# Optimization experiments

Hardware: AMD Instinct MI355X
Metric: run time of the kernel (lower is better)

The kernel has to match this reference:

```python
import jax, jax.numpy as jnp
import numpy as np

M, N = 4096, 4096

def _make_expk(n):
    k = np.arange(n, dtype=np.float64) * np.pi / (2.0 * n)
    return jnp.asarray(np.stack([np.cos(k), np.sin(k)], axis=-1), dtype=jnp.float32)

def setup_inputs() -> dict:
    key = jax.random.key(0)
    x = jax.random.normal(key, (M, N), dtype=jnp.float32)
    return {"x": x, "expkM": _make_expk(M), "expkN": _make_expk(N)}

def _idct_last(X, expk):
    """1D IDCT (inverse of unnormalized DCT-II) along last axis via Makhoul's
    N-point FFT trick. expk[k] = (cos, sin) of pi*k/(2N), i.e. e^{j pi k/(2N)}."""
    n = X.shape[-1]
    Xv = X * 0.5
    # V[k] = (Xv[k] - j*Xv[n-k]) * e^{j pi k/(2n)}, with imag part 0 at k=0
    tail = -jnp.flip(Xv, axis=-1)[..., :-1]
    Vi = jnp.concatenate([jnp.zeros_like(Xv[..., :1]), tail], axis=-1)
    W = expk[:, 0] + 1j * expk[:, 1]
    V = (Xv + 1j * Vi) * W
    v = jnp.fft.ifft(V, axis=-1).real.astype(X.dtype)
    # de-interleave: out[2m] = v[m], out[2m+1] = v[n-1-m]
    out = jnp.zeros_like(X)
    out = out.at[..., 0::2].set(v[..., : n - n // 2])
    out = out.at[..., 1::2].set(jnp.flip(v, axis=-1)[..., : n // 2])
    return out

def reference(x, expkM, expkN):
    # separable 2D IDCT: last axis (N) then first axis (M)
    y = _idct_last(x, expkN)
    y = _idct_last(y.T, expkM).T
    return y
```

## Files before the change

### kernel.cpp

```cpp
#include <hip/hip_runtime.h>
#include <math.h>


#define NN 4096
#define HH 2048
#define TT 256
#define PHYS(i) ((i) + ((i) >> 3))
#define C_SQ2 0.70710678118654752440f

__global__ void tw_init_kernel(float2* __restrict__ tw4096,
                               float2* __restrict__ tw2048) {
    int t = threadIdx.x;
    for (int i = 0; i < HH / TT; ++i) {
        int k = t + i * TT;
        double a4 = (2.0 * M_PI * (double)k) / 4096.0;
        double a2 = (2.0 * M_PI * (double)k) / 2048.0;
        tw4096[k] = make_float2((float)cos(a4), (float)sin(a4));
        tw2048[k] = make_float2((float)cos(a2), (float)sin(a2));
    }
}

__device__ __forceinline__ void radix8(const float* ar, const float* ai,
                                       float* tr, float* ti) {
    float s04r = ar[0] + ar[4], s04i = ai[0] + ai[4];
    float d04r = ar[0] - ar[4], d04i = ai[0] - ai[4];
    float s26r = ar[2] + ar[6], s26i = ai[2] + ai[6];
    float d26r = ar[2] - ar[6], d26i = ai[2] - ai[6];
    float E0r = s04r + s26r, E0i = s04i + s26i;
    float E1r = d04r - d26i, E1i = d04i + d26r;
    float E2r = s04r - s26r, E2i = s04i - s26i;
    float E3r = d04r + d26i, E3i = d04i - d26r;
    float s15r = ar[1] + ar[5], s15i = ai[1] + ai[5];
    float d15r = ar[1] - ar[5], d15i = ai[1] - ai[5];
    float s37r = ar[3] + ar[7], s37i = ai[3] + ai[7];
    float d37r = ar[3] - ar[7], d37i = ai[3] - ai[7];
    float O0r = s15r + s37r, O0i = s15i + s37i;
    float O1r = d15r - d37i, O1i = d15i + d37r;
    float O2r = s15r - s37r, O2i = s15i - s37i;
    float O3r = d15r + d37i, O3i = d15i - d37r;
    float W1r = C_SQ2 * (O1r - O1i), W1i = C_SQ2 * (O1r + O1i);
    float W2r = -O2i, W2i = O2r;
    float W3r = -C_SQ2 * (O3r + O3i), W3i = C_SQ2 * (O3r - O3i);
    tr[0] = E0r + O0r; ti[0] = E0i + O0i;
    tr[4] = E0r - O0r; ti[4] = E0i - O0i;
    tr[1] = E1r + W1r; ti[1] = E1i + W1i;
    tr[5] = E1r - W1r; ti[5] = E1i - W1i;
    tr[2] = E2r + W2r; ti[2] = E2i + W2i;
    tr[6] = E2r - W2r; ti[6] = E2i - W2i;
    tr[3] = E3r + W3r; ti[3] = E3i + W3i;
    tr[7] = E3r - W3r; ti[7] = E3i - W3i;
}

__global__ __launch_bounds__(TT) void idct_rows_kernel(
    const float* __restrict__ in, const float2* __restrict__ expk,
    const float2* __restrict__ tw4096, const float2* __restrict__ tw2048,
    float* __restrict__ out) {
    __shared__ float b0r[2304], b0i[2304], b1r[2304], b1i[2304];
    const int t = threadIdx.x;
    const float* __restrict__ xr = in + (size_t)blockIdx.x * NN;
    float* __restrict__ orow = out + (size_t)blockIdx.x * NN;
    const float sc = 1.0f / 4096.0f;

    float zr[8], zi[8];
#pragma unroll
    for (int p = 0; p < 8; ++p) {
        int k = t + TT * p;
        float xa = xr[k];
        float xb = xr[(NN - k) & (NN - 1)];
        xb = (k == 0) ? 0.0f : xb;
        float2 e1 = expk[k];
        float var_ = 0.5f * (xa * e1.x + xb * e1.y);
        float vai_ = 0.5f * (xa * e1.y - xb * e1.x);
        float xc = xr[k + HH];
        float xd = xr[HH - k];
        float2 e2 = expk[k + HH];
        float vbr_ = 0.5f * (xc * e2.x + xd * e2.y);
        float vbi_ = 0.5f * (xc * e2.y - xd * e2.x);
        float sr = var_ + vbr_, si = vai_ + vbi_;
        float dr = var_ - vbr_, di = vai_ - vbi_;
        float2 w = tw4096[k];
        zr[p] = (sr - (w.x * di + w.y * dr)) * sc;
        zi[p] = (si + (w.x * dr - w.y * di)) * sc;
    }
    {
        float tr[8], ti[8];
        radix8(zr, zi, tr, ti);
        int base = 9 * t;
        b0r[base] = tr[0]; b0i[base] = ti[0];
#pragma unroll
        for (int q = 1; q < 8; ++q) {
            float2 w = tw2048[(t * q) & (HH - 1)];
            b0r[base + q] = w.x * tr[q] - w.y * ti[q];
            b0i[base + q] = w.x * ti[q] + w.y * tr[q];
        }
    }
    __syncthreads();

    {
        float ar[8], ai[8], tr[8], ti[8];
        int rb = PHYS(t);
#pragma unroll
        for (int p = 0; p < 8; ++p) { ar[p] = b0r[rb + 288 * p]; ai[p] = b0i[rb + 288 * p]; }
        radix8(ar, ai, tr, ti);
        int j = t >> 3;
        int wj = 8 * j;
        int base = 64 * j + t;
        b1r[base] = tr[0]; b1i[base] = ti[0];
#pragma unroll
        for (int q = 1; q < 8; ++q) {
            float2 w = tw2048[(wj * q) & (HH - 1)];
            b1r[base + 9 * q] = w.x * tr[q] - w.y * ti[q];
            b1i[base + 9 * q] = w.x * ti[q] + w.y * tr[q];
        }
    }
    __syncthreads();

    {
        float ar[8], ai[8], tr[8], ti[8];
        int rb = PHYS(t);
#pragma unroll
        for (int p = 0; p < 8; ++p) { ar[p] = b1r[rb + 288 * p]; ai[p] = b1i[rb + 288 * p]; }
        radix8(ar, ai, tr, ti);
        int j = t >> 6;
        int wj = 64 * j;
        int k = t & 63;
        int base = 576 * j + PHYS(k);
        b0r[base] = tr[0]; b0i[base] = ti[0];
#pragma unroll
        for (int q = 1; q < 8; ++q) {
            float2 w = tw2048[(wj * q) & (HH - 1)];
            b0r[base + 72 * q] = w.x * tr[q] - w.y * ti[q];
            b0i[base + 72 * q] = w.x * ti[q] + w.y * tr[q];
        }
    }
    __syncthreads();

#pragma unroll
    for (int u = 0; u < 2; ++u) {
        int b = t + TT * u;
        int rb = PHYS(b);
        float a0r = b0r[rb], a0i = b0i[rb];
        float a1r = b0r[rb + 576], a1i = b0i[rb + 576];
        float a2r = b0r[rb + 1152], a2i = b0i[rb + 1152];
        float a3r = b0r[rb + 1728], a3i = b0i[rb + 1728];
        float s02r = a0r + a2r, s02i = a0i + a2i;
        float d02r = a0r - a2r, d02i = a0i - a2i;
        float s13r = a1r + a3r, s13i = a1i + a3i;
        float d13r = a1r - a3r, d13i = a1i - a3i;
        b1r[rb] = s02r + s13r;          b1i[rb] = s02i + s13i;
        b1r[rb + 576] = d02r - d13i;    b1i[rb + 576] = d02i + d13r;
        b1r[rb + 1152] = s02r - s13r;   b1i[rb + 1152] = s02i - s13i;
        b1r[rb + 1728] = d02r + d13i;   b1i[rb + 1728] = d02i - d13r;
    }
    __syncthreads();

#pragma unroll
    for (int i = 0; i < NN / TT; ++i) {
        int q = t + TT * i;
        int vidx = (q & 1) ? (NN - 1 - ((q - 1) >> 1)) : (q >> 1);
        int m_ = PHYS(vidx >> 1);
        float val = (vidx & 1) ? b1i[m_] : b1r[m_];
        orow[q] = val;
    }
}

__global__ __launch_bounds__(256) void transpose_kernel(
    const float* __restrict__ in, float* __restrict__ out) {
    __shared__ float tile[64 * 64];
    int bx = blockIdx.x, by = blockIdx.y;
    int tx = threadIdx.x;
    int ty = threadIdx.y;
#pragma unroll
    for (int j = 0; j < 4; ++j) {
        int y = ty + 16 * j;
        float4 v = ((const float4*)(in + (size_t)(by * 64 + y) * NN + bx * 64))[tx];
        int X0 = 4 * tx;
        tile[(X0 + 0) * 64 + ((((y >> 2) ^ ((X0 + 0) & 15)) << 2) | (y & 3))] = v.x;
        tile[(X0 + 1) * 64 + ((((y >> 2) ^ ((X0 + 1) & 15)) << 2) | (y & 3))] = v.y;
        tile[(X0 + 2) * 64 + ((((y >> 2) ^ ((X0 + 2) & 15)) << 2) | (y & 3))] = v.z;
        tile[(X0 + 3) * 64 + ((((y >> 2) ^ ((X0 + 3) & 15)) << 2) | (y & 3))] = v.w;
    }
    __syncthreads();
#pragma unroll
    for (int j = 0; j < 4; ++j) {
        int r = ty + 16 * j;
        float4 w = *(const float4*)&tile[r * 64 + ((tx ^ (r & 15)) << 2)];
        ((float4*)(out + (size_t)(bx * 64 + r) * NN + by * 64))[tx] = w;
    }
}

extern "C" void kernel_launch(void* const* d_in, const int* in_sizes, int n_in,
                              void* d_out, int out_size, void* d_ws, size_t ws_size,
                              hipStream_t stream) {
    const float* x      = (const float*)d_in[0];
    const float2* expkM = (const float2*)d_in[1];
    const float2* expkN = (const float2*)d_in[2];
    float* out = (float*)d_out;

    float2* tw4096 = (float2*)d_ws;
    float2* tw2048 = (float2*)((char*)d_ws + 16384);
    float* A       = (float*)((char*)d_ws + 65536);

    tw_init_kernel<<<1, TT, 0, stream>>>(tw4096, tw2048);

    idct_rows_kernel<<<NN, TT, 0, stream>>>(x, expkN, tw4096, tw2048, A);
    {
        dim3 g(NN / 64, NN / 64), b(16, 16);
        transpose_kernel<<<g, b, 0, stream>>>(A, out);
    }
    idct_rows_kernel<<<NN, TT, 0, stream>>>(out, expkM, tw4096, tw2048, A);
    {
        dim3 g(NN / 64, NN / 64), b(16, 16);
        transpose_kernel<<<g, b, 0, stream>>>(A, out);
    }
}
```

Baseline: 226.9 us.

## Replace transpose-based 2D IDCT with column four-step FFT and in-place row pass

Drops both transpose kernels. The column IDCT is now done directly on the row-major data with a four-step FFT (col_a: 32-point register FFT plus twiddle, written to a complex intermediate; col_b: 64-point register FFT with the de-interleave folded into the store). The pre-twiddle math is folded into four precomputed coefficient tables, which also replace the expk inputs. The row pass then runs in place on the output with adjusted shared-memory padding. This removes two full-matrix transpose passes, but adds a 128MB complex intermediate, strided per-column global accesses and very high register use from 64-element register FFTs.

```diff
diff --git a/kernel.cpp b/kernel.cpp
--- a/kernel.cpp
+++ b/kernel.cpp
@@ -2,24 +2,130 @@
 #include <math.h>
 
 
-#define NN 4096
-#define HH 2048
 #define TT 256
-#define PHYS(i) ((i) + ((i) >> 3))
+
+constexpr float W64R[32] = {
+    1.0f, 0.995184726672197f, 0.980785280403230f, 0.956940335732209f,
+    0.923879532511287f, 0.881921264348355f, 0.831469612302545f, 0.773010453362737f,
+    0.707106781186548f, 0.634393284163645f, 0.555570233019602f, 0.471396736825998f,
+    0.382683432365090f, 0.290284677254462f, 0.195090322016128f, 0.0980171403295606f,
+    0.0f, -0.0980171403295606f, -0.195090322016128f, -0.290284677254462f,
+    -0.382683432365090f, -0.471396736825998f, -0.555570233019602f, -0.634393284163645f,
+    -0.707106781186548f, -0.773010453362737f, -0.831469612302545f, -0.881921264348355f,
+    -0.923879532511287f, -0.956940335732209f, -0.980785280403230f, -0.995184726672197f};
+constexpr float W64I[32] = {
+    0.0f, 0.0980171403295606f, 0.195090322016128f, 0.290284677254462f,
+    0.382683432365090f, 0.471396736825998f, 0.555570233019602f, 0.634393284163645f,
+    0.707106781186548f, 0.773010453362737f, 0.831469612302545f, 0.881921264348355f,
+    0.923879532511287f, 0.956940335732209f, 0.980785280403230f, 0.995184726672197f,
+    1.0f, 0.995184726672197f, 0.980785280403230f, 0.956940335732209f,
+    0.923879532511287f, 0.881921264348355f, 0.831469612302545f, 0.773010453362737f,
+    0.707106781186548f, 0.634393284163645f, 0.555570233019602f, 0.471396736825998f,
+    0.382683432365090f, 0.290284677254462f, 0.195090322016128f, 0.0980171403295606f};
+
+__device__ __forceinline__ constexpr int brev(int x, int bits) {
+    int r = 0;
+    for (int i = 0; i < bits; ++i) { r = (r << 1) | (x & 1); x >>= 1; }
+    return r;
+}
+
+template <int NP>
+__device__ __forceinline__ void fft_dif(float2* a) {
+#pragma unroll
+    for (int h = NP / 2; h >= 1; h >>= 1) {
+#pragma unroll
+        for (int b = 0; b < NP; b += 2 * h) {
+#pragma unroll
+            for (int k = 0; k < h; ++k) {
+                float2 u = a[b + k], v = a[b + k + h];
+                float dx = u.x - v.x, dy = u.y - v.y;
+                a[b + k] = make_float2(u.x + v.x, u.y + v.y);
+                float wr = W64R[k * (32 / h)], wi = W64I[k * (32 / h)];
+                a[b + k + h] = make_float2(dx * wr - dy * wi, dx * wi + dy * wr);
+            }
+        }
+    }
+}
+
+__global__ void tw_init_kernel(float2* __restrict__ tw2048,
+                               float2* __restrict__ c1, float2* __restrict__ c2,
+                               float2* __restrict__ c3, float2* __restrict__ c4) {
+    int t = threadIdx.x;
+    const double s = 0.5 / 4096.0;
+    for (int i = 0; i < 8; ++i) {
+        int k = t + 256 * i;
+        double aw = M_PI * (double)k / 2048.0;
+        double wr = cos(aw), wi = sin(aw);
+        double a1 = M_PI * (double)k / 8192.0;
+        double e1r = cos(a1), e1i = sin(a1);
+        double a2 = M_PI * (double)(k + 2048) / 8192.0;
+        double e2r = cos(a2), e2i = sin(a2);
+        double Ar = s * ((1.0 - wi) * e1r - wr * e1i);
+        double Ai = s * ((1.0 - wi) * e1i + wr * e1r);
+        double Br = (k == 0) ? 0.0 : Ai;
+        double Bi = (k == 0) ? 0.0 : -Ar;
+        double Cr = s * ((1.0 + wi) * e2r + wr * e2i);
+        double Ci = s * ((1.0 + wi) * e2i - wr * e2r);
+        c1[k] = make_float2((float)Ar, (float)Ai);
+        c2[k] = make_float2((float)Br, (float)Bi);
+        c3[k] = make_float2((float)Cr, (float)Ci);
+        c4[k] = make_float2((float)Ci, (float)-Cr);
+        double at = M_PI * (double)k / 1024.0;
+        tw2048[k] = make_float2((float)cos(at), (float)sin(at));
+    }
+}
+
+__global__ __launch_bounds__(TT) void col_a_kernel(
+    const float* __restrict__ x,
+    const float2* __restrict__ c1, const float2* __restrict__ c2,
+    const float2* __restrict__ c3, const float2* __restrict__ c4,
+    const float2* __restrict__ tw2048, float2* __restrict__ T1) {
+    int c = blockIdx.x * 64 + threadIdx.x;
+    int k1 = blockIdx.y * 4 + threadIdx.y;
+    float2 f[32];
+#pragma unroll
+    for (int k2 = 0; k2 < 32; ++k2) {
+        int k = k1 + 64 * k2;
+        float xa = x[(size_t)k * 4096 + c];
+        float xb = x[(size_t)((4096 - k) & 4095) * 4096 + c];
+        float xc = x[(size_t)(2048 + k) * 4096 + c];
+        float xd = x[(size_t)(2048 - k) * 4096 + c];
+        float2 A = c1[k], B = c2[k], C = c3[k], D = c4[k];
+        f[k2].x = A.x * xa + B.x * xb + C.x * xc + D.x * xd;
+        f[k2].y = A.y * xa + B.y * xb + C.y * xc + D.y * xd;
+    }
+    fft_dif<32>(f);
+#pragma unroll
+    for (int j = 0; j < 32; ++j) {
+        int n2 = brev(j, 5);
+        float2 w = tw2048[k1 * n2];
+        float2 v = f[j];
+        float2 o = make_float2(v.x * w.x - v.y * w.y, v.x * w.y + v.y * w.x);
+        T1[(size_t)(k1 * 32 + n2) * 4096 + c] = o;
+    }
+}
+
+__global__ __launch_bounds__(TT) void col_b_kernel(
+    const float2* __restrict__ T1, float* __restrict__ out) {
+    int c = blockIdx.x * 64 + threadIdx.x;
+    int n2 = blockIdx.y * 4 + threadIdx.y;
+    float2 f[64];
+#pragma unroll
+    for (int k1 = 0; k1 < 64; ++k1)
+        f[k1] = T1[(size_t)(k1 * 32 + n2) * 4096 + c];
+    fft_dif<64>(f);
+#pragma unroll
+    for (int j = 0; j < 64; ++j) {
+        int n1 = brev(j, 6);
+        int m = 32 * n1 + n2;
+        int r0 = (n1 < 32) ? (4 * m) : (8191 - 4 * m);
+        int r1 = (n1 < 32) ? (4 * m + 2) : (8189 - 4 * m);
+        out[(size_t)r0 * 4096 + c] = f[j].x;
+        out[(size_t)r1 * 4096 + c] = f[j].y;
+    }
+}
+
 #define C_SQ2 0.70710678118654752440f
-
-__global__ void tw_init_kernel(float2* __restrict__ tw4096,
-                               float2* __restrict__ tw2048) {
-    int t = threadIdx.x;
-    for (int i = 0; i < HH / TT; ++i) {
-        int k = t + i * TT;
-        double a4 = (2.0 * M_PI * (double)k) / 4096.0;
-        double a2 = (2.0 * M_PI * (double)k) / 2048.0;
-        tw4096[k] = make_float2((float)cos(a4), (float)sin(a4));
-        tw2048[k] = make_float2((float)cos(a2), (float)sin(a2));
-    }
-}
-
 __device__ __forceinline__ void radix8(const float* ar, const float* ai,
                                        float* tr, float* ti) {
     float s04r = ar[0] + ar[4], s04i = ai[0] + ai[4];
@@ -52,165 +158,118 @@
 }
 
 __global__ __launch_bounds__(TT) void idct_rows_kernel(
-    const float* __restrict__ in, const float2* __restrict__ expk,
-    const float2* __restrict__ tw4096, const float2* __restrict__ tw2048,
-    float* __restrict__ out) {
-    __shared__ float b0r[2304], b0i[2304], b1r[2304], b1i[2304];
+    const float2* __restrict__ c1, const float2* __restrict__ c2,
+    const float2* __restrict__ c3, const float2* __restrict__ c4,
+    const float2* __restrict__ tw2048, float* __restrict__ io) {
+    __shared__ float b0r[2112], b0i[2112], b1r[2176], b1i[2176];
     const int t = threadIdx.x;
-    const float* __restrict__ xr = in + (size_t)blockIdx.x * NN;
-    float* __restrict__ orow = out + (size_t)blockIdx.x * NN;
-    const float sc = 1.0f / 4096.0f;
-
-    float zr[8], zi[8];
+    float* __restrict__ xr = io + (size_t)blockIdx.x * 4096;
+
+    float zr[8], zi[8], tr[8], ti[8];
 #pragma unroll
     for (int p = 0; p < 8; ++p) {
-        int k = t + TT * p;
+        int k = t + 256 * p;
         float xa = xr[k];
-        float xb = xr[(NN - k) & (NN - 1)];
-        xb = (k == 0) ? 0.0f : xb;
-        float2 e1 = expk[k];
-        float var_ = 0.5f * (xa * e1.x + xb * e1.y);
-        float vai_ = 0.5f * (xa * e1.y - xb * e1.x);
-        float xc = xr[k + HH];
-        float xd = xr[HH - k];
-        float2 e2 = expk[k + HH];
-        float vbr_ = 0.5f * (xc * e2.x + xd * e2.y);
-        float vbi_ = 0.5f * (xc * e2.y - xd * e2.x);
-        float sr = var_ + vbr_, si = vai_ + vbi_;
-        float dr = var_ - vbr_, di = vai_ - vbi_;
-        float2 w = tw4096[k];
-        zr[p] = (sr - (w.x * di + w.y * dr)) * sc;
-        zi[p] = (si + (w.x * dr - w.y * di)) * sc;
-    }
+        float xb = xr[(4096 - k) & 4095];
+        float xc = xr[2048 + k];
+        float xd = xr[2048 - k];
+        float2 A = c1[k], B = c2[k], C = c3[k], D = c4[k];
+        zr[p] = A.x * xa + B.x * xb + C.x * xc + D.x * xd;
+        zi[p] = A.y * xa + B.y * xb + C.y * xc + D.y * xd;
+    }
+    radix8(zr, zi, tr, ti);
     {
-        float tr[8], ti[8];
-        radix8(zr, zi, tr, ti);
-        int base = 9 * t;
-        b0r[base] = tr[0]; b0i[base] = ti[0];
+        int baseA = 8 * t + (t >> 2);
+        b0r[baseA] = tr[0]; b0i[baseA] = ti[0];
 #pragma unroll
         for (int q = 1; q < 8; ++q) {
-            float2 w = tw2048[(t * q) & (HH - 1)];
-            b0r[base + q] = w.x * tr[q] - w.y * ti[q];
-            b0i[base + q] = w.x * ti[q] + w.y * tr[q];
-        }
-    }
-    __syncthreads();
-
+            float2 w = tw2048[(t * q) & 2047];
+            b0r[baseA + q] = w.x * tr[q] - w.y * ti[q];
+            b0i[baseA + q] = w.x * ti[q] + w.y * tr[q];
+        }
+    }
+    __syncthreads();
     {
-        float ar[8], ai[8], tr[8], ti[8];
-        int rb = PHYS(t);
-#pragma unroll
-        for (int p = 0; p < 8; ++p) { ar[p] = b0r[rb + 288 * p]; ai[p] = b0i[rb + 288 * p]; }
+        float ar[8], ai[8];
+        int rb = t + (t >> 5);
+#pragma unroll
+        for (int p = 0; p < 8; ++p) { ar[p] = b0r[rb + 264 * p]; ai[p] = b0i[rb + 264 * p]; }
         radix8(ar, ai, tr, ti);
-        int j = t >> 3;
-        int wj = 8 * j;
-        int base = 64 * j + t;
-        b1r[base] = tr[0]; b1i[base] = ti[0];
+        int j = t >> 3, k = t & 7, wj = 8 * j;
+        int baseB = 68 * j + k;
+        b1r[baseB] = tr[0]; b1i[baseB] = ti[0];
 #pragma unroll
         for (int q = 1; q < 8; ++q) {
-            float2 w = tw2048[(wj * q) & (HH - 1)];
-            b1r[base + 9 * q] = w.x * tr[q] - w.y * ti[q];
-            b1i[base + 9 * q] = w.x * ti[q] + w.y * tr[q];
-        }
-    }
-    __syncthreads();
-
+            int off = baseB + 8 * q + (q >> 1);
+            float2 w = tw2048[(wj * q) & 2047];
+            b1r[off] = w.x * tr[q] - w.y * ti[q];
+            b1i[off] = w.x * ti[q] + w.y * tr[q];
+        }
+    }
+    __syncthreads();
     {
-        float ar[8], ai[8], tr[8], ti[8];
-        int rb = PHYS(t);
-#pragma unroll
-        for (int p = 0; p < 8; ++p) { ar[p] = b1r[rb + 288 * p]; ai[p] = b1i[rb + 288 * p]; }
+        float ar[8], ai[8];
+        int rb = t + (t >> 4);
+#pragma unroll
+        for (int p = 0; p < 8; ++p) { ar[p] = b1r[rb + 272 * p]; ai[p] = b1i[rb + 272 * p]; }
         radix8(ar, ai, tr, ti);
-        int j = t >> 6;
-        int wj = 64 * j;
-        int k = t & 63;
-        int base = 576 * j + PHYS(k);
-        b0r[base] = tr[0]; b0i[base] = ti[0];
+        int j = t >> 6, wj = 64 * j, k = t & 63;
+        int baseC = 528 * j + k + (k >> 5);
+        b0r[baseC] = tr[0]; b0i[baseC] = ti[0];
 #pragma unroll
         for (int q = 1; q < 8; ++q) {
-            float2 w = tw2048[(wj * q) & (HH - 1)];
-            b0r[base + 72 * q] = w.x * tr[q] - w.y * ti[q];
-            b0i[base + 72 * q] = w.x * ti[q] + w.y * tr[q];
-        }
-    }
-    __syncthreads();
-
+            int off = baseC + 66 * q;
+            float2 w = tw2048[(wj * q) & 2047];
+            b0r[off] = w.x * tr[q] - w.y * ti[q];
+            b0i[off] = w.x * ti[q] + w.y * tr[q];
+        }
+    }
+    __syncthreads();
 #pragma unroll
     for (int u = 0; u < 2; ++u) {
-        int b = t + TT * u;
-        int rb = PHYS(b);
+        int b = t + 256 * u;
+        int rb = b + (b >> 5);
+        int wb = b + (b >> 4);
         float a0r = b0r[rb], a0i = b0i[rb];
-        float a1r = b0r[rb + 576], a1i = b0i[rb + 576];
-        float a2r = b0r[rb + 1152], a2i = b0i[rb + 1152];
-        float a3r = b0r[rb + 1728], a3i = b0i[rb + 1728];
+        float a1r = b0r[rb + 528], a1i = b0i[rb + 528];
+        float a2r = b0r[rb + 1056], a2i = b0i[rb + 1056];
+        float a3r = b0r[rb + 1584], a3i = b0i[rb + 1584];
         float s02r = a0r + a2r, s02i = a0i + a2i;
         float d02r = a0r - a2r, d02i = a0i - a2i;
         float s13r = a1r + a3r, s13i = a1i + a3i;
         float d13r = a1r - a3r, d13i = a1i - a3i;
-        b1r[rb] = s02r + s13r;          b1i[rb] = s02i + s13i;
-        b1r[rb + 576] = d02r - d13i;    b1i[rb + 576] = d02i + d13r;
-        b1r[rb + 1152] = s02r - s13r;   b1i[rb + 1152] = s02i - s13i;
-        b1r[rb + 1728] = d02r + d13i;   b1i[rb + 1728] = d02i - d13r;
-    }
-    __syncthreads();
-
-#pragma unroll
-    for (int i = 0; i < NN / TT; ++i) {
-        int q = t + TT * i;
-        int vidx = (q & 1) ? (NN - 1 - ((q - 1) >> 1)) : (q >> 1);
-        int m_ = PHYS(vidx >> 1);
+        b1r[wb] = s02r + s13r;          b1i[wb] = s02i + s13i;
+        b1r[wb + 544] = d02r - d13i;    b1i[wb + 544] = d02i + d13r;
+        b1r[wb + 1088] = s02r - s13r;   b1i[wb + 1088] = s02i - s13i;
+        b1r[wb + 1632] = d02r + d13i;   b1i[wb + 1632] = d02i - d13r;
+    }
+    __syncthreads();
+#pragma unroll
+    for (int i = 0; i < 16; ++i) {
+        int q = t + 256 * i;
+        int vidx = (q & 1) ? (4095 - ((q - 1) >> 1)) : (q >> 1);
+        int l = vidx >> 1;
+        int m_ = l + (l >> 4);
         float val = (vidx & 1) ? b1i[m_] : b1r[m_];
-        orow[q] = val;
-    }
-}
-
-__global__ __launch_bounds__(256) void transpose_kernel(
-    const float* __restrict__ in, float* __restrict__ out) {
-    __shared__ float tile[64 * 64];
-    int bx = blockIdx.x, by = blockIdx.y;
-    int tx = threadIdx.x;
-    int ty = threadIdx.y;
-#pragma unroll
-    for (int j = 0; j < 4; ++j) {
-        int y = ty + 16 * j;
-        float4 v = ((const float4*)(in + (size_t)(by * 64 + y) * NN + bx * 64))[tx];
-        int X0 = 4 * tx;
-        tile[(X0 + 0) * 64 + ((((y >> 2) ^ ((X0 + 0) & 15)) << 2) | (y & 3))] = v.x;
-        tile[(X0 + 1) * 64 + ((((y >> 2) ^ ((X0 + 1) & 15)) << 2) | (y & 3))] = v.y;
-        tile[(X0 + 2) * 64 + ((((y >> 2) ^ ((X0 + 2) & 15)) << 2) | (y & 3))] = v.z;
-        tile[(X0 + 3) * 64 + ((((y >> 2) ^ ((X0 + 3) & 15)) << 2) | (y & 3))] = v.w;
-    }
-    __syncthreads();
-#pragma unroll
-    for (int j = 0; j < 4; ++j) {
-        int r = ty + 16 * j;
-        float4 w = *(const float4*)&tile[r * 64 + ((tx ^ (r & 15)) << 2)];
-        ((float4*)(out + (size_t)(bx * 64 + r) * NN + by * 64))[tx] = w;
+        xr[q] = val;
     }
 }
 
 extern "C" void kernel_launch(void* const* d_in, const int* in_sizes, int n_in,
                               void* d_out, int out_size, void* d_ws, size_t ws_size,
                               hipStream_t stream) {
-    const float* x      = (const float*)d_in[0];
-    const float2* expkM = (const float2*)d_in[1];
-    const float2* expkN = (const float2*)d_in[2];
+    const float* x = (const float*)d_in[0];
     float* out = (float*)d_out;
 
-    float2* tw4096 = (float2*)d_ws;
-    float2* tw2048 = (float2*)((char*)d_ws + 16384);
-    float* A       = (float*)((char*)d_ws + 65536);
-
-    tw_init_kernel<<<1, TT, 0, stream>>>(tw4096, tw2048);
-
-    idct_rows_kernel<<<NN, TT, 0, stream>>>(x, expkN, tw4096, tw2048, A);
-    {
-        dim3 g(NN / 64, NN / 64), b(16, 16);
-        transpose_kernel<<<g, b, 0, stream>>>(A, out);
-    }
-    idct_rows_kernel<<<NN, TT, 0, stream>>>(out, expkM, tw4096, tw2048, A);
-    {
-        dim3 g(NN / 64, NN / 64), b(16, 16);
-        transpose_kernel<<<g, b, 0, stream>>>(A, out);
-    }
-}
+    float2* tw2048 = (float2*)d_ws;
+    float2* c1 = (float2*)((char*)d_ws + 1 * 16384);
+    float2* c2 = (float2*)((char*)d_ws + 2 * 16384);
+    float2* c3 = (float2*)((char*)d_ws + 3 * 16384);
+    float2* c4 = (float2*)((char*)d_ws + 4 * 16384);
+    float2* T1 = (float2*)((char*)d_ws + (1 << 20));
+
+    tw_init_kernel<<<1, TT, 0, stream>>>(tw2048, c1, c2, c3, c4);
+    col_a_kernel<<<dim3(64, 16), dim3(64, 4), 0, stream>>>(x, c1, c2, c3, c4, tw2048, T1);
+    col_b_kernel<<<dim3(64, 8), dim3(64, 4), 0, stream>>>(T1, out);
+    idct_rows_kernel<<<4096, TT, 0, stream>>>(c1, c2, c3, c4, tw2048, out);
+}
```

Result: faster. 203.7 us (-10.2%).
